# Performance work log

Hardware: AMD Instinct MI355X
Metric: run time of the kernel (lower is better)

The kernel has to match this reference:

```python
import jax, jax.numpy as jnp
import numpy as np

# --- model hyperparameters (match init_kwargs) ---
N_NODES = 128
IN_F = 3
H = 32            # hidden_node_size = output_node_size
HE = 64           # hidden_edge_size
OE = 32           # output_edge_size
N_MPS = 4
N_NODE_LAYERS = 2
ALPHA = 0.1       # leaky relu slope
E_IN = 2 * H + 2  # input_edge_size with intensity=True
BN_EPS = 1e-5


def _bn(x, gamma, beta):
    # BatchNorm1d in training mode: biased batch statistics over axis 0
    mu = jnp.mean(x, axis=0)
    var = jnp.var(x, axis=0)
    return gamma * (x - mu) * jax.lax.rsqrt(var + BN_EPS) + beta


def _lrelu(x):
    return jax.nn.leaky_relu(x, negative_slope=ALPHA)


def setup_inputs() -> dict:
    key = jax.random.key(0)
    ks = jax.random.split(key, 20)
    B = 64
    s = 0.05
    inp = {
        "x": jax.random.normal(ks[0], (B, N_NODES, IN_F), dtype=jnp.float32),
        # edge MLP (aggregate_hidden, aggregate), stacked over mp steps
        "Wah": jax.random.normal(ks[1], (N_MPS, E_IN, HE), dtype=jnp.float32) * s,
        "bah": jax.random.normal(ks[2], (N_MPS, HE), dtype=jnp.float32) * s,
        "Wa": jax.random.normal(ks[3], (N_MPS, HE, OE), dtype=jnp.float32) * s,
        "ba": jax.random.normal(ks[4], (N_MPS, OE), dtype=jnp.float32) * s,
        # edge batchnorm affine params
        "g_eh": jnp.ones((N_MPS, HE), dtype=jnp.float32),
        "b_eh": jnp.zeros((N_MPS, HE), dtype=jnp.float32),
        "g_e": jnp.ones((N_MPS, OE), dtype=jnp.float32),
        "b_e": jnp.zeros((N_MPS, OE), dtype=jnp.float32),
        # node update MLP: first layer (OE+H -> H), then (L-1) layers (H -> H)
        "Wn0": jax.random.normal(ks[5], (N_MPS, OE + H, H), dtype=jnp.float32) * s,
        "bn0": jax.random.normal(ks[6], (N_MPS, H), dtype=jnp.float32) * s,
        "Wn": jax.random.normal(ks[7], (N_MPS, N_NODE_LAYERS - 1, H, H), dtype=jnp.float32) * s,
        "bnn": jax.random.normal(ks[8], (N_MPS, N_NODE_LAYERS - 1, H), dtype=jnp.float32) * s,
        # node batchnorm affine params (one per node hidden layer)
        "g_n": jnp.ones((N_MPS, N_NODE_LAYERS, H), dtype=jnp.float32),
        "b_n": jnp.zeros((N_MPS, N_NODE_LAYERS, H), dtype=jnp.float32),
        # final update linear
        "Wu": jax.random.normal(ks[9], (N_MPS, H, H), dtype=jnp.float32) * s,
        "bu": jax.random.normal(ks[10], (N_MPS, H), dtype=jnp.float32) * s,
    }
    return inp


def reference(x, Wah, bah, Wa, ba, g_eh, b_eh, g_e, b_e, Wn0, bn0, Wn, bnn, g_n, b_n, Wu, bu):
    B, N, Fi = x.shape
    # pad input node features to hidden_node_size
    x = jnp.pad(x, ((0, 0), (0, 0), (0, H - Fi)))  # [B, N, H]
    for i in range(N_MPS):
        # dense all-pairs edge features: row (a,b) = [x_a, x_b, dist_ab, int_ab]
        x1 = jnp.broadcast_to(x[:, :, None, :], (B, N, N, H))  # sender varies on axis 1
        x2 = jnp.broadcast_to(x[:, None, :, :], (B, N, N, H))  # receiver varies on axis 2
        diff = x2[..., :-1] - x1[..., :-1] + 1e-12             # [B,N,N,H-1]
        dists = jnp.sqrt(jnp.sum(diff * diff, axis=-1, keepdims=True))
        int_diffs = 1.0 - (x2[..., -1:] - x1[..., -1:])
        A = jnp.concatenate([x1, x2, dists, int_diffs], axis=-1)
        A = A.reshape(B * N * N, E_IN)
        # edge MLP with batchnorm (training-mode stats); dropout p=0 (identity)
        A = _bn(_lrelu(A @ Wah[i] + bah[i]), g_eh[i], b_eh[i])
        A = _bn(_lrelu(A @ Wa[i] + ba[i]), g_e[i], b_e[i])
        # sum-aggregate over neighbors (axis 2)
        agg = jnp.sum(A.reshape(B, N, N, OE), axis=2)          # [B, N, OE]
        h = jnp.concatenate([agg, x], axis=-1).reshape(B * N, OE + H)
        # node update MLP
        h = _bn(_lrelu(h @ Wn0[i] + bn0[i]), g_n[i, 0], b_n[i, 0])
        for j in range(1, N_NODE_LAYERS):
            h = _bn(_lrelu(h @ Wn[i, j - 1] + bnn[i, j - 1]), g_n[i, j], b_n[i, j])
        x = jnp.tanh(h @ Wu[i] + bu[i]).reshape(B, N, H)
    return x
```

## Files before the change

kernel.cpp:

```cpp
#include <hip/hip_runtime.h>
#include <hip/hip_bf16.h>


#define ALPHA 0.1f
#define BN_EPS 1e-5f
#define LRELU(v) ((v) > 0.f ? (v) : ALPHA * (v))

typedef __attribute__((ext_vector_type(8))) short short8v;
typedef __attribute__((ext_vector_type(4))) float f32x4;

union U8 { short8v v; unsigned int u[4]; };

__device__ __forceinline__ unsigned short bf16rne(float f) {
    unsigned int u = __float_as_uint(f);
    unsigned int r = u + 0x7fffu + ((u >> 16) & 1u);
    return (unsigned short)(r >> 16);
}
__device__ __forceinline__ float bf16tof(unsigned short h) {
    return __uint_as_float(((unsigned int)h) << 16);
}
__device__ __forceinline__ void cvt8(const float* y, unsigned int* hu, unsigned int* lu) {
#pragma unroll
    for (int p = 0; p < 4; ++p) {
        unsigned int hpair;
        asm("v_cvt_pk_bf16_f32 %0, %1, %2" : "=v"(hpair) : "v"(y[2*p]), "v"(y[2*p+1]));
        const float h0 = __uint_as_float(hpair << 16);
        const float h1 = __uint_as_float(hpair & 0xffff0000u);
        unsigned int lpair;
        const float r0 = y[2*p] - h0;
        const float r1 = y[2*p+1] - h1;
        asm("v_cvt_pk_bf16_f32 %0, %1, %2" : "=v"(lpair) : "v"(r0), "v"(r1));
        hu[p] = hpair;
        lu[p] = lpair;
    }
}

__global__ __launch_bounds__(128) void k_pad_prep(const float* __restrict__ x,
                                                  const float* __restrict__ W1,
                                                  const float* __restrict__ b1,
                                                  float* __restrict__ xc,
                                                  float* __restrict__ P1,
                                                  float* __restrict__ P2,
                                                  float2* __restrict__ nbuf) {
    __shared__ float w1s[384];
    __shared__ float b1s[64];
    const int tid = threadIdx.x;
    for (int u = tid; u < 384; u += 128) {
        const int r = u >> 6, c = u & 63;
        const int srow = (r < 3) ? r : (32 + r - 3);
        w1s[u] = W1[srow * 64 + c];
    }
    if (tid < 64) b1s[tid] = b1[tid];
    const int row = blockIdx.x * 128 + tid;
    const float x0 = x[row * 3 + 0], x1 = x[row * 3 + 1], x2 = x[row * 3 + 2];
    __syncthreads();
    float4* xp = (float4*)(xc + row * 32);
    xp[0] = make_float4(x0, x1, x2, 0.f);
    const float4 z4 = make_float4(0.f, 0.f, 0.f, 0.f);
#pragma unroll
    for (int u = 1; u < 8; ++u) xp[u] = z4;
    nbuf[row] = make_float2(x0 * x0 + x1 * x1 + x2 * x2, 0.f);
    float* p1p = P1 + row * 64;
    float* p2p = P2 + row * 64;
#pragma unroll
    for (int c = 0; c < 64; ++c) {
        p1p[c] = b1s[c] + x0 * w1s[c] + x1 * w1s[64 + c] + x2 * w1s[128 + c];
        p2p[c] = x0 * w1s[192 + c] + x1 * w1s[256 + c] + x2 * w1s[320 + c];
    }
}

__global__ __launch_bounds__(256) void k_edge1(const float* __restrict__ xc,
                                               const float2* __restrict__ nbuf,
                                               const float* __restrict__ P1,
                                               const float* __restrict__ P2,
                                               const float* __restrict__ W1,
                                               float* __restrict__ stA) {
    __shared__ float xs[128 * 33];
    __shared__ float ddot[1024];
    __shared__ float2 nls[128];
    __shared__ float p1s[512];
    __shared__ float red[256];
    const int tid = threadIdx.x;
    const int b = blockIdx.x >> 4;
    const int ibase = (blockIdx.x & 15) * 8;
    const float* xg = xc + b * 4096;
    for (int u = tid; u < 4096; u += 256) xs[(u >> 5) * 33 + (u & 31)] = xg[u];
    if (tid < 128) nls[tid] = nbuf[b * 128 + tid];
    for (int u = tid; u < 512; u += 256)
        p1s[u] = P1[(b * 128 + ibase + (u >> 6)) * 64 + (u & 63)];
    __syncthreads();
    {
        const int il = tid >> 5, jb = tid & 31;
        const float* xi = &xs[(ibase + il) * 33];
        float xi_r[31];
#pragma unroll
        for (int k = 0; k < 31; ++k) xi_r[k] = xi[k];
        for (int q = 0; q < 4; ++q) {
            const int j = jb + 32 * q;
            const float* xj = &xs[j * 33];
            float d = 0.f;
#pragma unroll
            for (int k = 0; k < 31; ++k) d = fmaf(xi_r[k], xj[k], d);
            ddot[il * 128 + j] = d;
        }
    }
    __syncthreads();
    const int w = tid >> 6, l = tid & 63;
    const int tq = tid & 127;
    const int ch = (tid >> 7) * 32;
    const float2 nj = nls[tq];
    float4 p2v[8], wav[8], wbv[8];
    {
        const float* p2r = P2 + (b * 128 + tq) * 64 + ch;
        const float* war = W1 + 64 * 64 + ch;
        const float* wbr = W1 + 65 * 64 + ch;
#pragma unroll
        for (int u = 0; u < 8; ++u) {
            p2v[u] = *(const float4*)(p2r + u * 4);
            wav[u] = *(const float4*)(war + u * 4);
            wbv[u] = *(const float4*)(wbr + u * 4);
        }
    }
    float sum[32], sq[32];
#pragma unroll
    for (int k = 0; k < 32; ++k) { sum[k] = 0.f; sq[k] = 0.f; }
#pragma unroll 1
    for (int c = 0; c < 8; ++c) {
        const float2 ni = nls[ibase + c];
        const float dot = ddot[c * 128 + tq];
        const float dist = sqrtf(fmaxf(ni.x + nj.x - 2.f * dot, 0.f));
        const float itf = 1.f - (nj.y - ni.y);
        const float* p1r = &p1s[c * 64 + ch];
#pragma unroll
        for (int u = 0; u < 8; ++u) {
            const float4 p1v = *(const float4*)(p1r + u * 4);
            const float4 p2q = p2v[u];
            const float4 wa = wav[u];
            const float4 wb = wbv[u];
            float y0 = fmaf(itf, wb.x, fmaf(dist, wa.x, p1v.x + p2q.x));
            float y1 = fmaf(itf, wb.y, fmaf(dist, wa.y, p1v.y + p2q.y));
            float y2 = fmaf(itf, wb.z, fmaf(dist, wa.z, p1v.z + p2q.z));
            float y3 = fmaf(itf, wb.w, fmaf(dist, wa.w, p1v.w + p2q.w));
            y0 = LRELU(y0); y1 = LRELU(y1); y2 = LRELU(y2); y3 = LRELU(y3);
            sum[4*u+0] += y0; sq[4*u+0] += y0 * y0;
            sum[4*u+1] += y1; sq[4*u+1] += y1 * y1;
            sum[4*u+2] += y2; sq[4*u+2] += y2 * y2;
            sum[4*u+3] += y3; sq[4*u+3] += y3 * y3;
        }
    }
    {
        const int b5 = (l >> 5) & 1;
#pragma unroll
        for (int i = 0; i < 32; ++i) {
            const float keep = b5 ? sq[i] : sum[i];
            const float send = b5 ? sum[i] : sq[i];
            sum[i] = keep + __shfl_xor(send, 32, 64);
        }
        const int b4 = (l >> 4) & 1;
#pragma unroll
        for (int i = 0; i < 16; ++i) {
            const float keep = b4 ? sum[i + 16] : sum[i];
            const float send = b4 ? sum[i] : sum[i + 16];
            sum[i] = keep + __shfl_xor(send, 16, 64);
        }
        const int b3 = (l >> 3) & 1;
#pragma unroll
        for (int i = 0; i < 8; ++i) {
            const float keep = b3 ? sum[i + 8] : sum[i];
            const float send = b3 ? sum[i] : sum[i + 8];
            sum[i] = keep + __shfl_xor(send, 8, 64);
        }
        const int b2 = (l >> 2) & 1;
#pragma unroll
        for (int i = 0; i < 4; ++i) {
            const float keep = b2 ? sum[i + 4] : sum[i];
            const float send = b2 ? sum[i] : sum[i + 4];
            sum[i] = keep + __shfl_xor(send, 4, 64);
        }
        const int b1 = (l >> 1) & 1;
#pragma unroll
        for (int i = 0; i < 2; ++i) {
            const float keep = b1 ? sum[i + 2] : sum[i];
            const float send = b1 ? sum[i] : sum[i + 2];
            sum[i] = keep + __shfl_xor(send, 2, 64);
        }
        const int b0 = l & 1;
        {
            const float keep = b0 ? sum[1] : sum[0];
            const float send = b0 ? sum[0] : sum[1];
            sum[0] = keep + __shfl_xor(send, 1, 64);
        }
    }
    red[w * 64 + l] = sum[0];
    __syncthreads();
    if (tid < 128) {
        const int half = tid >> 6;
        const int l2 = tid & 63;
        const float val = red[half * 128 + l2] + red[half * 128 + 64 + l2];
        const int col = half * 32 + (l2 & 31);
        const int idx = (l2 < 32) ? col : (64 + col);
        atomicAdd(stA + idx, val);
    }
}

__global__ __launch_bounds__(256) void k_edge2(const float* __restrict__ xc,
                                               const float2* __restrict__ nbuf,
                                               const float* __restrict__ P1,
                                               const float* __restrict__ P2,
                                               const float* __restrict__ W1,
                                               const float* __restrict__ W2,
                                               const float* __restrict__ b2g,
                                               const float* __restrict__ g1,
                                               const float* __restrict__ bt1,
                                               const float* __restrict__ stA,
                                               float* __restrict__ stB,
                                               float* __restrict__ aggp) {
    __shared__ __align__(16) char smem_u[16896];
    __shared__ float ddot[1024];
    __shared__ float2 nls[128];
    __shared__ unsigned short wfbs[4096];
    __shared__ float s1s[64], t1s[64];
    __shared__ float p1s[512];
    __shared__ float part[256];
    __shared__ float b2ps[32];
    __shared__ float aggl[256];
    __shared__ float sqil[256];
    float* xs = (float*)smem_u;
    float* cbAll = (float*)smem_u;
    const int tid = threadIdx.x;
    const int b = blockIdx.x >> 4;
    const int ibase = (blockIdx.x & 15) * 8;
    const float* xg = xc + b * 4096;
    for (int u = tid; u < 4096; u += 256) xs[(u >> 5) * 33 + (u & 31)] = xg[u];
    if (tid < 128) nls[tid] = nbuf[b * 128 + tid];
    for (int u = tid; u < 512; u += 256)
        p1s[u] = P1[(b * 128 + ibase + (u >> 6)) * 64 + (u & 63)];
    if (tid < 64) {
        const float ic = 1.f / 1048576.f;
        const float mu = stA[tid] * ic;
        const float var = stA[64 + tid] * ic - mu * mu;
        const float sv = g1[tid] * rsqrtf(var + BN_EPS);
        s1s[tid] = sv;
        t1s[tid] = bt1[tid] - mu * sv;
    }
    __syncthreads();
    {
        const int il = tid >> 5, jb = tid & 31;
        const float* xi = &xs[(ibase + il) * 33];
        float xi_r[31];
#pragma unroll
        for (int k = 0; k < 31; ++k) xi_r[k] = xi[k];
        for (int q = 0; q < 4; ++q) {
            const int j = jb + 32 * q;
            const float* xj = &xs[j * 33];
            float d = 0.f;
#pragma unroll
            for (int k = 0; k < 31; ++k) d = fmaf(xi_r[k], xj[k], d);
            ddot[il * 128 + j] = d;
        }
    }
    {
        const int ks2n = tid >> 6, L = tid & 63;
        const int ks = ks2n >> 1, n = ks2n & 1;
#pragma unroll
        for (int e = 0; e < 8; ++e) {
            const int k = (L >> 4) * 8 + e + 32 * ks;
            const int col = n * 16 + (L & 15);
            const float wv = W2[k * 32 + col] * s1s[k];
            const unsigned short hi = bf16rne(wv);
            const unsigned short lo = bf16rne(wv - bf16tof(hi));
            wfbs[(ks2n * 64 + L) * 8 + e] = hi;
            wfbs[2048 + (ks2n * 64 + L) * 8 + e] = lo;
        }
    }
    {
        const int colp = tid & 31, kg2 = tid >> 5;
        float p = 0.f;
#pragma unroll
        for (int e = 0; e < 8; ++e) {
            const int k = kg2 * 8 + e;
            p = fmaf(t1s[k], W2[k * 32 + colp], p);
        }
        part[kg2 * 32 + colp] = p;
    }
    __syncthreads();
    if (tid < 32) {
        float acc = b2g[tid];
#pragma unroll
        for (int g = 0; g < 8; ++g) acc += part[g * 32 + tid];
        b2ps[tid] = acc;
    }
    const int w = tid >> 6, l = tid & 63;
    short8v bfh[2][2], bfl[2][2];
#pragma unroll
    for (int ks = 0; ks < 2; ++ks)
#pragma unroll
        for (int n = 0; n < 2; ++n) {
            bfh[ks][n] = *(const short8v*)(wfbs + ((ks * 2 + n) * 64 + l) * 8);
            bfl[ks][n] = *(const short8v*)(wfbs + 2048 + ((ks * 2 + n) * 64 + l) * 8);
        }
    __syncthreads();
    const float b2p0 = b2ps[l & 15];
    const float b2p1 = b2ps[16 + (l & 15)];
    const int kb = (l >> 4) * 8;
    const int lb4 = (l >> 4) & 1;
    const int lb5 = (l >> 5) & 1;
    const float* wab = W1 + 64 * 64;
    const float* wbb = W1 + 65 * 64;
    const float4 waA0 = *(const float4*)(wab + kb);
    const float4 waA1 = *(const float4*)(wab + kb + 4);
    const float4 waB0 = *(const float4*)(wab + 32 + kb);
    const float4 waB1 = *(const float4*)(wab + 32 + kb + 4);
    const float4 wbA0 = *(const float4*)(wbb + kb);
    const float4 wbA1 = *(const float4*)(wbb + kb + 4);
    const float4 wbB0 = *(const float4*)(wbb + 32 + kb);
    const float4 wbB1 = *(const float4*)(wbb + 32 + kb + 4);
    const int jrow0 = (w * 2 + 0) * 16 + (l & 15);
    const int jrow1 = (w * 2 + 1) * 16 + (l & 15);
    const float2 nj0 = nls[jrow0];
    const float2 nj1 = nls[jrow1];
    float4 p2r0v[4], p2r1v[4];
    {
        const float* p2b0 = P2 + (b * 128 + jrow0) * 64;
        const float* p2b1 = P2 + (b * 128 + jrow1) * 64;
        p2r0v[0] = *(const float4*)(p2b0 + kb);
        p2r0v[1] = *(const float4*)(p2b0 + kb + 4);
        p2r0v[2] = *(const float4*)(p2b0 + 32 + kb);
        p2r0v[3] = *(const float4*)(p2b0 + 32 + kb + 4);
        p2r1v[0] = *(const float4*)(p2b1 + kb);
        p2r1v[1] = *(const float4*)(p2b1 + kb + 4);
        p2r1v[2] = *(const float4*)(p2b1 + 32 + kb);
        p2r1v[3] = *(const float4*)(p2b1 + 32 + kb + 4);
    }

#pragma unroll 1
    for (int c = 0; c < 8; ++c) {
        const float2 ni = nls[ibase + c];
        const float* p1b = &p1s[c * 64];
        const float4 p1A0 = *(const float4*)(p1b + kb);
        const float4 p1A1 = *(const float4*)(p1b + kb + 4);
        const float4 p1B0 = *(const float4*)(p1b + 32 + kb);
        const float4 p1B1 = *(const float4*)(p1b + 32 + kb + 4);
        float accg = 0.f;
        {
            const float dot = ddot[c * 128 + jrow0];
            const float dist = sqrtf(fmaxf(ni.x + nj0.x - 2.f * dot, 0.f));
            const float itf = 1.f - (nj0.y - ni.y);
            const float4 p20 = p2r0v[0];
            const float4 p21 = p2r0v[1];
            const float4 p22 = p2r0v[2];
            const float4 p23 = p2r0v[3];
            float ya[8], yb[8];
            ya[0] = LRELU(fmaf(itf, wbA0.x, fmaf(dist, waA0.x, p1A0.x + p20.x)));
            ya[1] = LRELU(fmaf(itf, wbA0.y, fmaf(dist, waA0.y, p1A0.y + p20.y)));
            ya[2] = LRELU(fmaf(itf, wbA0.z, fmaf(dist, waA0.z, p1A0.z + p20.z)));
            ya[3] = LRELU(fmaf(itf, wbA0.w, fmaf(dist, waA0.w, p1A0.w + p20.w)));
            ya[4] = LRELU(fmaf(itf, wbA1.x, fmaf(dist, waA1.x, p1A1.x + p21.x)));
            ya[5] = LRELU(fmaf(itf, wbA1.y, fmaf(dist, waA1.y, p1A1.y + p21.y)));
            ya[6] = LRELU(fmaf(itf, wbA1.z, fmaf(dist, waA1.z, p1A1.z + p21.z)));
            ya[7] = LRELU(fmaf(itf, wbA1.w, fmaf(dist, waA1.w, p1A1.w + p21.w)));
            yb[0] = LRELU(fmaf(itf, wbB0.x, fmaf(dist, waB0.x, p1B0.x + p22.x)));
            yb[1] = LRELU(fmaf(itf, wbB0.y, fmaf(dist, waB0.y, p1B0.y + p22.y)));
            yb[2] = LRELU(fmaf(itf, wbB0.z, fmaf(dist, waB0.z, p1B0.z + p22.z)));
            yb[3] = LRELU(fmaf(itf, wbB0.w, fmaf(dist, waB0.w, p1B0.w + p22.w)));
            yb[4] = LRELU(fmaf(itf, wbB1.x, fmaf(dist, waB1.x, p1B1.x + p23.x)));
            yb[5] = LRELU(fmaf(itf, wbB1.y, fmaf(dist, waB1.y, p1B1.y + p23.y)));
            yb[6] = LRELU(fmaf(itf, wbB1.z, fmaf(dist, waB1.z, p1B1.z + p23.z)));
            yb[7] = LRELU(fmaf(itf, wbB1.w, fmaf(dist, waB1.w, p1B1.w + p23.w)));
            U8 a0h, a0l, a1h, a1l;
            cvt8(ya, a0h.u, a0l.u);
            cvt8(yb, a1h.u, a1l.u);
            f32x4 acc0 = {0.f, 0.f, 0.f, 0.f};
            f32x4 acc1 = {0.f, 0.f, 0.f, 0.f};
            acc0 = __builtin_amdgcn_mfma_f32_16x16x32_bf16(a0h.v, bfh[0][0], acc0, 0, 0, 0);
            acc0 = __builtin_amdgcn_mfma_f32_16x16x32_bf16(a0h.v, bfl[0][0], acc0, 0, 0, 0);
            acc0 = __builtin_amdgcn_mfma_f32_16x16x32_bf16(a0l.v, bfh[0][0], acc0, 0, 0, 0);
            acc0 = __builtin_amdgcn_mfma_f32_16x16x32_bf16(a1h.v, bfh[1][0], acc0, 0, 0, 0);
            acc0 = __builtin_amdgcn_mfma_f32_16x16x32_bf16(a1h.v, bfl[1][0], acc0, 0, 0, 0);
            acc0 = __builtin_amdgcn_mfma_f32_16x16x32_bf16(a1l.v, bfh[1][0], acc0, 0, 0, 0);
            acc1 = __builtin_amdgcn_mfma_f32_16x16x32_bf16(a0h.v, bfh[0][1], acc1, 0, 0, 0);
            acc1 = __builtin_amdgcn_mfma_f32_16x16x32_bf16(a0h.v, bfl[0][1], acc1, 0, 0, 0);
            acc1 = __builtin_amdgcn_mfma_f32_16x16x32_bf16(a0l.v, bfh[0][1], acc1, 0, 0, 0);
            acc1 = __builtin_amdgcn_mfma_f32_16x16x32_bf16(a1h.v, bfh[1][1], acc1, 0, 0, 0);
            acc1 = __builtin_amdgcn_mfma_f32_16x16x32_bf16(a1h.v, bfl[1][1], acc1, 0, 0, 0);
            acc1 = __builtin_amdgcn_mfma_f32_16x16x32_bf16(a1l.v, bfh[1][1], acc1, 0, 0, 0);
            float s0 = 0.f, q0 = 0.f, s1 = 0.f, q1 = 0.f;
#pragma unroll
            for (int r4 = 0; r4 < 4; ++r4) {
                const float z0 = LRELU(acc0[r4] + b2p0);
                const float z1 = LRELU(acc1[r4] + b2p1);
                s0 += z0; q0 += z0 * z0;
                s1 += z1; q1 += z1 * z1;
            }
            float sA = lb4 ? s1 : s0;
            float sB = lb4 ? s0 : s1;
            float qA = lb4 ? q1 : q0;
            float qB = lb4 ? q0 : q1;
            sA += __shfl_xor(sB, 16, 64);
            qA += __shfl_xor(qB, 16, 64);
            float vA = lb5 ? qA : sA;
            float vB = lb5 ? sA : qA;
            vA += __shfl_xor(vB, 32, 64);
            accg = vA;
        }
        {
            const float dot = ddot[c * 128 + jrow1];
            const float dist = sqrtf(fmaxf(ni.x + nj1.x - 2.f * dot, 0.f));
            const float itf = 1.f - (nj1.y - ni.y);
            const float4 p20 = p2r1v[0];
            const float4 p21 = p2r1v[1];
            const float4 p22 = p2r1v[2];
            const float4 p23 = p2r1v[3];
            float ya[8], yb[8];
            ya[0] = LRELU(fmaf(itf, wbA0.x, fmaf(dist, waA0.x, p1A0.x + p20.x)));
            ya[1] = LRELU(fmaf(itf, wbA0.y, fmaf(dist, waA0.y, p1A0.y + p20.y)));
            ya[2] = LRELU(fmaf(itf, wbA0.z, fmaf(dist, waA0.z, p1A0.z + p20.z)));
            ya[3] = LRELU(fmaf(itf, wbA0.w, fmaf(dist, waA0.w, p1A0.w + p20.w)));
            ya[4] = LRELU(fmaf(itf, wbA1.x, fmaf(dist, waA1.x, p1A1.x + p21.x)));
            ya[5] = LRELU(fmaf(itf, wbA1.y, fmaf(dist, waA1.y, p1A1.y + p21.y)));
            ya[6] = LRELU(fmaf(itf, wbA1.z, fmaf(dist, waA1.z, p1A1.z + p21.z)));
            ya[7] = LRELU(fmaf(itf, wbA1.w, fmaf(dist, waA1.w, p1A1.w + p21.w)));
            yb[0] = LRELU(fmaf(itf, wbB0.x, fmaf(dist, waB0.x, p1B0.x + p22.x)));
            yb[1] = LRELU(fmaf(itf, wbB0.y, fmaf(dist, waB0.y, p1B0.y + p22.y)));
            yb[2] = LRELU(fmaf(itf, wbB0.z, fmaf(dist, waB0.z, p1B0.z + p22.z)));
            yb[3] = LRELU(fmaf(itf, wbB0.w, fmaf(dist, waB0.w, p1B0.w + p22.w)));
            yb[4] = LRELU(fmaf(itf, wbB1.x, fmaf(dist, waB1.x, p1B1.x + p23.x)));
            yb[5] = LRELU(fmaf(itf, wbB1.y, fmaf(dist, waB1.y, p1B1.y + p23.y)));
            yb[6] = LRELU(fmaf(itf, wbB1.z, fmaf(dist, waB1.z, p1B1.z + p23.z)));
            yb[7] = LRELU(fmaf(itf, wbB1.w, fmaf(dist, waB1.w, p1B1.w + p23.w)));
            U8 a0h, a0l, a1h, a1l;
            cvt8(ya, a0h.u, a0l.u);
            cvt8(yb, a1h.u, a1l.u);
            f32x4 acc0 = {0.f, 0.f, 0.f, 0.f};
            f32x4 acc1 = {0.f, 0.f, 0.f, 0.f};
            acc0 = __builtin_amdgcn_mfma_f32_16x16x32_bf16(a0h.v, bfh[0][0], acc0, 0, 0, 0);
            acc0 = __builtin_amdgcn_mfma_f32_16x16x32_bf16(a0h.v, bfl[0][0], acc0, 0, 0, 0);
            acc0 = __builtin_amdgcn_mfma_f32_16x16x32_bf16(a0l.v, bfh[0][0], acc0, 0, 0, 0);
            acc0 = __builtin_amdgcn_mfma_f32_16x16x32_bf16(a1h.v, bfh[1][0], acc0, 0, 0, 0);
            acc0 = __builtin_amdgcn_mfma_f32_16x16x32_bf16(a1h.v, bfl[1][0], acc0, 0, 0, 0);
            acc0 = __builtin_amdgcn_mfma_f32_16x16x32_bf16(a1l.v, bfh[1][0], acc0, 0, 0, 0);
            acc1 = __builtin_amdgcn_mfma_f32_16x16x32_bf16(a0h.v, bfh[0][1], acc1, 0, 0, 0);
            acc1 = __builtin_amdgcn_mfma_f32_16x16x32_bf16(a0h.v, bfl[0][1], acc1, 0, 0, 0);
            acc1 = __builtin_amdgcn_mfma_f32_16x16x32_bf16(a0l.v, bfh[0][1], acc1, 0, 0, 0);
            acc1 = __builtin_amdgcn_mfma_f32_16x16x32_bf16(a1h.v, bfh[1][1], acc1, 0, 0, 0);
            acc1 = __builtin_amdgcn_mfma_f32_16x16x32_bf16(a1h.v, bfl[1][1], acc1, 0, 0, 0);
            acc1 = __builtin_amdgcn_mfma_f32_16x16x32_bf16(a1l.v, bfh[1][1], acc1, 0, 0, 0);
            float s0 = 0.f, q0 = 0.f, s1 = 0.f, q1 = 0.f;
#pragma unroll
            for (int r4 = 0; r4 < 4; ++r4) {
                const float z0 = LRELU(acc0[r4] + b2p0);
                const float z1 = LRELU(acc1[r4] + b2p1);
                s0 += z0; q0 += z0 * z0;
                s1 += z1; q1 += z1 * z1;
            }
            float sA = lb4 ? s1 : s0;
            float sB = lb4 ? s0 : s1;
            float qA = lb4 ? q1 : q0;
            float qB = lb4 ? q0 : q1;
            sA += __shfl_xor(sB, 16, 64);
            qA += __shfl_xor(qB, 16, 64);
            float vA = lb5 ? qA : sA;
            float vB = lb5 ? sA : qA;
            vA += __shfl_xor(vB, 32, 64);
            accg += vA;
        }
        cbAll[c * 256 + w * 64 + lb5 * 32 + lb4 * 16 + (l & 15)] = accg;
    }
    __syncthreads();
    {
        const int c2 = tid >> 5, col = tid & 31;
        const float* base = cbAll + c2 * 256;
        const float s = base[col] + base[64 + col] + base[128 + col] + base[192 + col];
        const float qq = base[32 + col] + base[96 + col] + base[160 + col] + base[224 + col];
        aggp[(b * 128 + ibase + c2) * 32 + col] = s;
        aggl[c2 * 32 + col] = s;
        sqil[c2 * 32 + col] = qq;
    }
    __syncthreads();
    if (tid < 32) {
        float s = 0.f, qq = 0.f;
#pragma unroll
        for (int il3 = 0; il3 < 8; ++il3) { s += aggl[il3 * 32 + tid]; qq += sqil[il3 * 32 + tid]; }
        atomicAdd(stB + tid, s);
        atomicAdd(stB + 32 + tid, qq);
    }
}

__device__ __forceinline__ void gbar(unsigned int* ctr, unsigned int target) {
    __syncthreads();
    if (threadIdx.x == 0) {
        __hip_atomic_fetch_add(ctr, 1u, __ATOMIC_ACQ_REL, __HIP_MEMORY_SCOPE_AGENT);
        while (__hip_atomic_load(ctr, __ATOMIC_ACQUIRE, __HIP_MEMORY_SCOPE_AGENT) < target) {
            __builtin_amdgcn_s_sleep(2);
        }
    }
    __syncthreads();
}

__global__ __launch_bounds__(256) void k_nodeF(
    const float* __restrict__ aggp, const float* __restrict__ xc,
    const float* __restrict__ W0, const float* __restrict__ b0,
    const float* __restrict__ stB, const float* __restrict__ g2, const float* __restrict__ bt2,
    const float* __restrict__ W1m, const float* __restrict__ b1m,
    float* __restrict__ stC, const float* __restrict__ gC, const float* __restrict__ btC,
    const float* __restrict__ W2m, const float* __restrict__ b2m,
    float* __restrict__ stD, const float* __restrict__ gD, const float* __restrict__ btD,
    float* __restrict__ xout,
    const float* __restrict__ W1n, const float* __restrict__ b1n,
    float* __restrict__ P1, float* __restrict__ P2, float2* __restrict__ nbuf,
    unsigned int* __restrict__ bar, int doPrep)
{
    __shared__ float w0s[2048];
    __shared__ float wms[1024];
    __shared__ float wus[1024];
    __shared__ float w1s[4096];
    __shared__ float b0s[32], s2s[32], t2s[32];
    __shared__ float bms[32], sCs[32], tCs[32];
    __shared__ float bus[32], sDs[32], tDs[32];
    __shared__ float b1s[64];
    __shared__ float red[256];
    const int tid = threadIdx.x;
    const int row = blockIdx.x * 256 + tid;
    for (int k = tid; k < 2048; k += 256) w0s[k] = W0[k];
    for (int k = tid; k < 1024; k += 256) { wms[k] = W1m[k]; wus[k] = W2m[k]; }
    if (doPrep) {
        for (int k = tid; k < 4096; k += 256) w1s[k] = W1n[k];
        if (tid < 64) b1s[tid] = b1n[tid];
    }
    if (tid < 32) {
        b0s[tid] = b0[tid]; bms[tid] = b1m[tid]; bus[tid] = b2m[tid];
        const float ic = 1.f / 1048576.f;
        const float mu = stB[tid] * ic;
        const float var = stB[32 + tid] * ic - mu * mu;
        const float sv = g2[tid] * rsqrtf(var + BN_EPS);
        s2s[tid] = sv; t2s[tid] = bt2[tid] - mu * sv;
    }
    __syncthreads();
    float h[64];
    {
        const float4* ap = (const float4*)(aggp + row * 32);
        const float4* xp = (const float4*)(xc + row * 32);
#pragma unroll
        for (int u = 0; u < 8; ++u) {
            const float4 a = ap[u];
            h[4*u+0] = fmaf(s2s[4*u+0], a.x, 128.f * t2s[4*u+0]);
            h[4*u+1] = fmaf(s2s[4*u+1], a.y, 128.f * t2s[4*u+1]);
            h[4*u+2] = fmaf(s2s[4*u+2], a.z, 128.f * t2s[4*u+2]);
            h[4*u+3] = fmaf(s2s[4*u+3], a.w, 128.f * t2s[4*u+3]);
            const float4 xv = xp[u];
            h[32+4*u+0] = xv.x; h[32+4*u+1] = xv.y; h[32+4*u+2] = xv.z; h[32+4*u+3] = xv.w;
        }
    }
    float v[32];
#pragma unroll
    for (int o0 = 0; o0 < 32; o0 += 4) {
        float z0 = b0s[o0], z1 = b0s[o0+1], z2 = b0s[o0+2], z3 = b0s[o0+3];
#pragma unroll
        for (int k = 0; k < 64; ++k) {
            const float4 wv = *(const float4*)&w0s[k * 32 + o0];
            const float hv = h[k];
            z0 = fmaf(hv, wv.x, z0); z1 = fmaf(hv, wv.y, z1);
            z2 = fmaf(hv, wv.z, z2); z3 = fmaf(hv, wv.w, z3);
        }
        v[o0] = LRELU(z0); v[o0+1] = LRELU(z1); v[o0+2] = LRELU(z2); v[o0+3] = LRELU(z3);
    }
    {
        float sarr[32], qarr[32];
#pragma unroll
        for (int o = 0; o < 32; ++o) {
            float s = v[o], q = v[o] * v[o];
#pragma unroll
            for (int m = 1; m < 64; m <<= 1) { s += __shfl_xor(s, m, 64); q += __shfl_xor(q, m, 64); }
            sarr[o] = s; qarr[o] = q;
        }
        const int lane = tid & 63, wid = tid >> 6;
        if (lane == 0) {
#pragma unroll
            for (int o = 0; o < 32; ++o) { red[wid * 64 + o] = sarr[o]; red[wid * 64 + 32 + o] = qarr[o]; }
        }
        __syncthreads();
        if (tid < 64) {
            const float t = red[tid] + red[64 + tid] + red[128 + tid] + red[192 + tid];
            atomicAdd(stC + tid, t);
        }
    }
    gbar(bar + 0, 32);
    if (tid < 32) {
        const float ic = 1.f / 8192.f;
        const float mu = __hip_atomic_load(stC + tid, __ATOMIC_RELAXED, __HIP_MEMORY_SCOPE_AGENT) * ic;
        const float sq = __hip_atomic_load(stC + 32 + tid, __ATOMIC_RELAXED, __HIP_MEMORY_SCOPE_AGENT) * ic;
        const float var = sq - mu * mu;
        const float sv = gC[tid] * rsqrtf(var + BN_EPS);
        sCs[tid] = sv; tCs[tid] = btC[tid] - mu * sv;
    }
    __syncthreads();
    float hh[32];
#pragma unroll
    for (int c = 0; c < 32; ++c) hh[c] = fmaf(sCs[c], v[c], tCs[c]);
    float v2[32];
#pragma unroll
    for (int o0 = 0; o0 < 32; o0 += 4) {
        float z0 = bms[o0], z1 = bms[o0+1], z2 = bms[o0+2], z3 = bms[o0+3];
#pragma unroll
        for (int k = 0; k < 32; ++k) {
            const float4 wv = *(const float4*)&wms[k * 32 + o0];
            const float hv = hh[k];
            z0 = fmaf(hv, wv.x, z0); z1 = fmaf(hv, wv.y, z1);
            z2 = fmaf(hv, wv.z, z2); z3 = fmaf(hv, wv.w, z3);
        }
        v2[o0] = LRELU(z0); v2[o0+1] = LRELU(z1); v2[o0+2] = LRELU(z2); v2[o0+3] = LRELU(z3);
    }
    {
        float sarr[32], qarr[32];
#pragma unroll
        for (int o = 0; o < 32; ++o) {
            float s = v2[o], q = v2[o] * v2[o];
#pragma unroll
            for (int m = 1; m < 64; m <<= 1) { s += __shfl_xor(s, m, 64); q += __shfl_xor(q, m, 64); }
            sarr[o] = s; qarr[o] = q;
        }
        const int lane = tid & 63, wid = tid >> 6;
        __syncthreads();
        if (lane == 0) {
#pragma unroll
            for (int o = 0; o < 32; ++o) { red[wid * 64 + o] = sarr[o]; red[wid * 64 + 32 + o] = qarr[o]; }
        }
        __syncthreads();
        if (tid < 64) {
            const float t = red[tid] + red[64 + tid] + red[128 + tid] + red[192 + tid];
            atomicAdd(stD + tid, t);
        }
    }
    gbar(bar + 1, 32);
    if (tid < 32) {
        const float ic = 1.f / 8192.f;
        const float mu = __hip_atomic_load(stD + tid, __ATOMIC_RELAXED, __HIP_MEMORY_SCOPE_AGENT) * ic;
        const float sq = __hip_atomic_load(stD + 32 + tid, __ATOMIC_RELAXED, __HIP_MEMORY_SCOPE_AGENT) * ic;
        const float var = sq - mu * mu;
        const float sv = gD[tid] * rsqrtf(var + BN_EPS);
        sDs[tid] = sv; tDs[tid] = btD[tid] - mu * sv;
    }
    __syncthreads();
    float h3[32];
#pragma unroll
    for (int c = 0; c < 32; ++c) h3[c] = fmaf(sDs[c], v2[c], tDs[c]);
    float xn[32];
    float* xp = xout + row * 32;
#pragma unroll
    for (int o0 = 0; o0 < 32; o0 += 4) {
        float z0 = bus[o0], z1 = bus[o0+1], z2 = bus[o0+2], z3 = bus[o0+3];
#pragma unroll
        for (int k = 0; k < 32; ++k) {
            const float4 wv = *(const float4*)&wus[k * 32 + o0];
            const float hv = h3[k];
            z0 = fmaf(hv, wv.x, z0); z1 = fmaf(hv, wv.y, z1);
            z2 = fmaf(hv, wv.z, z2); z3 = fmaf(hv, wv.w, z3);
        }
        xn[o0]   = tanhf(z0);
        xn[o0+1] = tanhf(z1);
        xn[o0+2] = tanhf(z2);
        xn[o0+3] = tanhf(z3);
        xp[o0] = xn[o0]; xp[o0+1] = xn[o0+1]; xp[o0+2] = xn[o0+2]; xp[o0+3] = xn[o0+3];
    }
    if (!doPrep) return;
    float n = 0.f;
#pragma unroll
    for (int k = 0; k < 31; ++k) n = fmaf(xn[k], xn[k], n);
    nbuf[row] = make_float2(n, xn[31]);
    float* p1p = P1 + row * 64;
    float* p2p = P2 + row * 64;
#pragma unroll
    for (int c0 = 0; c0 < 64; c0 += 4) {
        float a0 = b1s[c0], a1 = b1s[c0+1], a2 = b1s[c0+2], a3 = b1s[c0+3];
        float q0 = 0.f, q1 = 0.f, q2 = 0.f, q3 = 0.f;
#pragma unroll
        for (int k = 0; k < 32; ++k) {
            const float xv = xn[k];
            const float4 wa = *(const float4*)&w1s[k * 64 + c0];
            const float4 wb = *(const float4*)&w1s[(32 + k) * 64 + c0];
            a0 = fmaf(xv, wa.x, a0); a1 = fmaf(xv, wa.y, a1);
            a2 = fmaf(xv, wa.z, a2); a3 = fmaf(xv, wa.w, a3);
            q0 = fmaf(xv, wb.x, q0); q1 = fmaf(xv, wb.y, q1);
            q2 = fmaf(xv, wb.z, q2); q3 = fmaf(xv, wb.w, q3);
        }
        p1p[c0] = a0; p1p[c0+1] = a1; p1p[c0+2] = a2; p1p[c0+3] = a3;
        p2p[c0] = q0; p2p[c0+1] = q1; p2p[c0+2] = q2; p2p[c0+3] = q3;
    }
}

extern "C" void kernel_launch(void* const* d_in, const int* in_sizes, int n_in,
                              void* d_out, int out_size, void* d_ws, size_t ws_size,
                              hipStream_t stream) {
    const float* x    = (const float*)d_in[0];
    const float* Wah  = (const float*)d_in[1];
    const float* bah  = (const float*)d_in[2];
    const float* Wa   = (const float*)d_in[3];
    const float* ba   = (const float*)d_in[4];
    const float* g_eh = (const float*)d_in[5];
    const float* b_eh = (const float*)d_in[6];
    const float* g_e  = (const float*)d_in[7];
    const float* b_e  = (const float*)d_in[8];
    const float* Wn0  = (const float*)d_in[9];
    const float* bn0  = (const float*)d_in[10];
    const float* Wn   = (const float*)d_in[11];
    const float* bnn  = (const float*)d_in[12];
    const float* g_n  = (const float*)d_in[13];
    const float* b_n  = (const float*)d_in[14];
    const float* Wu   = (const float*)d_in[15];
    const float* bu   = (const float*)d_in[16];

    float* ws    = (float*)d_ws;
    float* xc    = ws;
    float* aggp  = ws + 262144;
    float* P1    = ws + 786432;
    float* P2    = ws + 1310720;
    float2* nbuf = (float2*)(ws + 1835008);
    float* stats = ws + 1867776;
    unsigned int* bar = (unsigned int*)(ws + 1869056);
    float* out   = (float*)d_out;

    hipMemsetAsync(stats, 0, (1280 + 16) * sizeof(float), stream);
    k_pad_prep<<<64, 128, 0, stream>>>(x, Wah, bah, xc, P1, P2, nbuf);

    for (int s = 0; s < 4; ++s) {
        const float* W1 = Wah + s * 66 * 64;
        const float* W2 = Wa + s * 64 * 32;
        const float* b2 = ba + s * 32;
        float* stA = stats + s * 320;
        float* stB = stA + 128;
        float* stC = stA + 192;
        float* stD = stA + 256;

        k_edge1<<<1024, 256, 0, stream>>>(xc, nbuf, P1, P2, W1, stA);
        k_edge2<<<1024, 256, 0, stream>>>(xc, nbuf, P1, P2, W1, W2, b2,
                                          g_eh + s * 64, b_eh + s * 64, stA, stB, aggp);
        k_nodeF<<<32, 256, 0, stream>>>(aggp, xc, Wn0 + s * 2048, bn0 + s * 32,
                                        stB, g_e + s * 32, b_e + s * 32,
                                        Wn + s * 1024, bnn + s * 32,
                                        stC, g_n + s * 64, b_n + s * 64,
                                        Wu + s * 1024, bu + s * 32,
                                        stD, g_n + s * 64 + 32, b_n + s * 64 + 32,
                                        (s == 3) ? out : xc,
                                        (s < 3) ? (Wah + (s + 1) * 66 * 64) : Wah,
                                        (s < 3) ? (bah + (s + 1) * 64) : bah,
                                        P1, P2, nbuf, bar + s * 2, (s < 3) ? 1 : 0);
    }
}
```

Baseline: 536.8 us.

## Split node kernel into 128 single-wave blocks with transpose-style butterfly reduction

The node-update kernel now launches 128 blocks of 64 threads instead of 32 blocks of 256, spreading the 8192 rows across more CUs. The per-column sum and sum-of-squares reduction is replaced by a recursive-halving butterfly across the wave, so each lane ends holding one of the 64 statistics. This cuts shuffles from 64×6 to 63 per lane and removes the shared-memory stage. In exchange, the grid barrier must now wait for 128 blocks and there are 4× more global atomics per stat. Each block also reloads the full weight set into LDS.

```diff
diff --git a/kernel.cpp b/kernel.cpp
--- a/kernel.cpp
+++ b/kernel.cpp
@@ -497,7 +497,7 @@
     __syncthreads();
 }
 
-__global__ __launch_bounds__(256) void k_nodeF(
+__global__ __launch_bounds__(64) void k_nodeF(
     const float* __restrict__ aggp, const float* __restrict__ xc,
     const float* __restrict__ W0, const float* __restrict__ b0,
     const float* __restrict__ stB, const float* __restrict__ g2, const float* __restrict__ bt2,
@@ -518,14 +518,13 @@
     __shared__ float bms[32], sCs[32], tCs[32];
     __shared__ float bus[32], sDs[32], tDs[32];
     __shared__ float b1s[64];
-    __shared__ float red[256];
     const int tid = threadIdx.x;
-    const int row = blockIdx.x * 256 + tid;
-    for (int k = tid; k < 2048; k += 256) w0s[k] = W0[k];
-    for (int k = tid; k < 1024; k += 256) { wms[k] = W1m[k]; wus[k] = W2m[k]; }
+    const int row = blockIdx.x * 64 + tid;
+    for (int k = tid; k < 2048; k += 64) w0s[k] = W0[k];
+    for (int k = tid; k < 1024; k += 64) { wms[k] = W1m[k]; wus[k] = W2m[k]; }
     if (doPrep) {
-        for (int k = tid; k < 4096; k += 256) w1s[k] = W1n[k];
-        if (tid < 64) b1s[tid] = b1n[tid];
+        for (int k = tid; k < 4096; k += 64) w1s[k] = W1n[k];
+        b1s[tid] = b1n[tid];
     }
     if (tid < 32) {
         b0s[tid] = b0[tid]; bms[tid] = b1m[tid]; bus[tid] = b2m[tid];
@@ -565,26 +564,53 @@
         v[o0] = LRELU(z0); v[o0+1] = LRELU(z1); v[o0+2] = LRELU(z2); v[o0+3] = LRELU(z3);
     }
     {
-        float sarr[32], qarr[32];
-#pragma unroll
-        for (int o = 0; o < 32; ++o) {
-            float s = v[o], q = v[o] * v[o];
-#pragma unroll
-            for (int m = 1; m < 64; m <<= 1) { s += __shfl_xor(s, m, 64); q += __shfl_xor(q, m, 64); }
-            sarr[o] = s; qarr[o] = q;
-        }
-        const int lane = tid & 63, wid = tid >> 6;
-        if (lane == 0) {
-#pragma unroll
-            for (int o = 0; o < 32; ++o) { red[wid * 64 + o] = sarr[o]; red[wid * 64 + 32 + o] = qarr[o]; }
-        }
-        __syncthreads();
-        if (tid < 64) {
-            const float t = red[tid] + red[64 + tid] + red[128 + tid] + red[192 + tid];
-            atomicAdd(stC + tid, t);
-        }
-    }
-    gbar(bar + 0, 32);
+        float su[32], qu[32];
+#pragma unroll
+        for (int o = 0; o < 32; ++o) { su[o] = v[o]; qu[o] = v[o] * v[o]; }
+        const int b5 = (tid >> 5) & 1;
+#pragma unroll
+        for (int i = 0; i < 32; ++i) {
+            const float keep = b5 ? qu[i] : su[i];
+            const float send = b5 ? su[i] : qu[i];
+            su[i] = keep + __shfl_xor(send, 32, 64);
+        }
+        const int b4 = (tid >> 4) & 1;
+#pragma unroll
+        for (int i = 0; i < 16; ++i) {
+            const float keep = b4 ? su[i + 16] : su[i];
+            const float send = b4 ? su[i] : su[i + 16];
+            su[i] = keep + __shfl_xor(send, 16, 64);
+        }
+        const int b3 = (tid >> 3) & 1;
+#pragma unroll
+        for (int i = 0; i < 8; ++i) {
+            const float keep = b3 ? su[i + 8] : su[i];
+            const float send = b3 ? su[i] : su[i + 8];
+            su[i] = keep + __shfl_xor(send, 8, 64);
+        }
+        const int b2 = (tid >> 2) & 1;
+#pragma unroll
+        for (int i = 0; i < 4; ++i) {
+            const float keep = b2 ? su[i + 4] : su[i];
+            const float send = b2 ? su[i] : su[i + 4];
+            su[i] = keep + __shfl_xor(send, 4, 64);
+        }
+        const int b1 = (tid >> 1) & 1;
+#pragma unroll
+        for (int i = 0; i < 2; ++i) {
+            const float keep = b1 ? su[i + 2] : su[i];
+            const float send = b1 ? su[i] : su[i + 2];
+            su[i] = keep + __shfl_xor(send, 2, 64);
+        }
+        const int b0b = tid & 1;
+        {
+            const float keep = b0b ? su[1] : su[0];
+            const float send = b0b ? su[0] : su[1];
+            su[0] = keep + __shfl_xor(send, 1, 64);
+        }
+        atomicAdd(stC + tid, su[0]);
+    }
+    gbar(bar + 0, 128);
     if (tid < 32) {
         const float ic = 1.f / 8192.f;
         const float mu = __hip_atomic_load(stC + tid, __ATOMIC_RELAXED, __HIP_MEMORY_SCOPE_AGENT) * ic;
@@ -611,27 +637,53 @@
         v2[o0] = LRELU(z0); v2[o0+1] = LRELU(z1); v2[o0+2] = LRELU(z2); v2[o0+3] = LRELU(z3);
     }
     {
-        float sarr[32], qarr[32];
-#pragma unroll
-        for (int o = 0; o < 32; ++o) {
-            float s = v2[o], q = v2[o] * v2[o];
-#pragma unroll
-            for (int m = 1; m < 64; m <<= 1) { s += __shfl_xor(s, m, 64); q += __shfl_xor(q, m, 64); }
-            sarr[o] = s; qarr[o] = q;
-        }
-        const int lane = tid & 63, wid = tid >> 6;
-        __syncthreads();
-        if (lane == 0) {
-#pragma unroll
-            for (int o = 0; o < 32; ++o) { red[wid * 64 + o] = sarr[o]; red[wid * 64 + 32 + o] = qarr[o]; }
-        }
-        __syncthreads();
-        if (tid < 64) {
-            const float t = red[tid] + red[64 + tid] + red[128 + tid] + red[192 + tid];
-            atomicAdd(stD + tid, t);
-        }
-    }
-    gbar(bar + 1, 32);
+        float su[32], qu[32];
+#pragma unroll
+        for (int o = 0; o < 32; ++o) { su[o] = v2[o]; qu[o] = v2[o] * v2[o]; }
+        const int b5 = (tid >> 5) & 1;
+#pragma unroll
+        for (int i = 0; i < 32; ++i) {
+            const float keep = b5 ? qu[i] : su[i];
+            const float send = b5 ? su[i] : qu[i];
+            su[i] = keep + __shfl_xor(send, 32, 64);
+        }
+        const int b4 = (tid >> 4) & 1;
+#pragma unroll
+        for (int i = 0; i < 16; ++i) {
+            const float keep = b4 ? su[i + 16] : su[i];
+            const float send = b4 ? su[i] : su[i + 16];
+            su[i] = keep + __shfl_xor(send, 16, 64);
+        }
+        const int b3 = (tid >> 3) & 1;
+#pragma unroll
+        for (int i = 0; i < 8; ++i) {
+            const float keep = b3 ? su[i + 8] : su[i];
+            const float send = b3 ? su[i] : su[i + 8];
+            su[i] = keep + __shfl_xor(send, 8, 64);
+        }
+        const int b2 = (tid >> 2) & 1;
+#pragma unroll
+        for (int i = 0; i < 4; ++i) {
+            const float keep = b2 ? su[i + 4] : su[i];
+            const float send = b2 ? su[i] : su[i + 4];
+            su[i] = keep + __shfl_xor(send, 4, 64);
+        }
+        const int b1 = (tid >> 1) & 1;
+#pragma unroll
+        for (int i = 0; i < 2; ++i) {
+            const float keep = b1 ? su[i + 2] : su[i];
+            const float send = b1 ? su[i] : su[i + 2];
+            su[i] = keep + __shfl_xor(send, 2, 64);
+        }
+        const int b0b = tid & 1;
+        {
+            const float keep = b0b ? su[1] : su[0];
+            const float send = b0b ? su[0] : su[1];
+            su[0] = keep + __shfl_xor(send, 1, 64);
+        }
+        atomicAdd(stD + tid, su[0]);
+    }
+    gbar(bar + 1, 128);
     if (tid < 32) {
         const float ic = 1.f / 8192.f;
         const float mu = __hip_atomic_load(stD + tid, __ATOMIC_RELAXED, __HIP_MEMORY_SCOPE_AGENT) * ic;
@@ -734,7 +786,7 @@
         k_edge1<<<1024, 256, 0, stream>>>(xc, nbuf, P1, P2, W1, stA);
         k_edge2<<<1024, 256, 0, stream>>>(xc, nbuf, P1, P2, W1, W2, b2,
                                           g_eh + s * 64, b_eh + s * 64, stA, stB, aggp);
-        k_nodeF<<<32, 256, 0, stream>>>(aggp, xc, Wn0 + s * 2048, bn0 + s * 32,
+        k_nodeF<<<128, 64, 0, stream>>>(aggp, xc, Wn0 + s * 2048, bn0 + s * 32,
                                         stB, g_e + s * 32, b_e + s * 32,
                                         Wn + s * 1024, bnn + s * 32,
                                         stC, g_n + s * 64, b_n + s * 64,
```

Result: no change. 542.4 us (+1.0%).

## Split each node row across four threads and launch four times more node blocks

Applied to the files above, without the earlier changes.

The fused node-update kernel now assigns each row to a group of four threads, each computing 8 output columns, and launches 128 blocks instead of 32. Full hidden vectors are rebuilt with intra-wave shuffles between layers. Batch-norm statistics are reduced with shorter shuffle trees before the atomics, and stores become float4. The aim is more CUs and more latency hiding for this serial per-row MLP chain. The cost is extra shuffles, redundant input loads, and a grid barrier that now spans 128 co-resident blocks.

```diff
diff --git a/kernel.cpp b/kernel.cpp
--- a/kernel.cpp
+++ b/kernel.cpp
@@ -520,7 +520,11 @@
     __shared__ float b1s[64];
     __shared__ float red[256];
     const int tid = threadIdx.x;
-    const int row = blockIdx.x * 256 + tid;
+    const int l = tid & 63, w = tid >> 6;
+    const int part = tid & 3;
+    const int row = blockIdx.x * 64 + (tid >> 2);
+    const int ob = part * 8;
+    const int gbase = l & ~3;
     for (int k = tid; k < 2048; k += 256) w0s[k] = W0[k];
     for (int k = tid; k < 1024; k += 256) { wms[k] = W1m[k]; wus[k] = W2m[k]; }
     if (doPrep) {
@@ -551,9 +555,10 @@
             h[32+4*u+0] = xv.x; h[32+4*u+1] = xv.y; h[32+4*u+2] = xv.z; h[32+4*u+3] = xv.w;
         }
     }
-    float v[32];
-#pragma unroll
-    for (int o0 = 0; o0 < 32; o0 += 4) {
+    float v[8];
+#pragma unroll
+    for (int oo = 0; oo < 8; oo += 4) {
+        const int o0 = ob + oo;
         float z0 = b0s[o0], z1 = b0s[o0+1], z2 = b0s[o0+2], z3 = b0s[o0+3];
 #pragma unroll
         for (int k = 0; k < 64; ++k) {
@@ -562,29 +567,32 @@
             z0 = fmaf(hv, wv.x, z0); z1 = fmaf(hv, wv.y, z1);
             z2 = fmaf(hv, wv.z, z2); z3 = fmaf(hv, wv.w, z3);
         }
-        v[o0] = LRELU(z0); v[o0+1] = LRELU(z1); v[o0+2] = LRELU(z2); v[o0+3] = LRELU(z3);
-    }
-    {
-        float sarr[32], qarr[32];
-#pragma unroll
-        for (int o = 0; o < 32; ++o) {
-            float s = v[o], q = v[o] * v[o];
-#pragma unroll
-            for (int m = 1; m < 64; m <<= 1) { s += __shfl_xor(s, m, 64); q += __shfl_xor(q, m, 64); }
-            sarr[o] = s; qarr[o] = q;
-        }
-        const int lane = tid & 63, wid = tid >> 6;
-        if (lane == 0) {
-#pragma unroll
-            for (int o = 0; o < 32; ++o) { red[wid * 64 + o] = sarr[o]; red[wid * 64 + 32 + o] = qarr[o]; }
-        }
-        __syncthreads();
-        if (tid < 64) {
-            const float t = red[tid] + red[64 + tid] + red[128 + tid] + red[192 + tid];
-            atomicAdd(stC + tid, t);
-        }
-    }
-    gbar(bar + 0, 32);
+        v[oo] = LRELU(z0); v[oo+1] = LRELU(z1); v[oo+2] = LRELU(z2); v[oo+3] = LRELU(z3);
+    }
+    {
+        float st[16];
+#pragma unroll
+        for (int i = 0; i < 8; ++i) { st[i] = v[i]; st[8 + i] = v[i] * v[i]; }
+#pragma unroll
+        for (int m = 4; m <= 32; m <<= 1) {
+#pragma unroll
+            for (int i = 0; i < 16; ++i) st[i] += __shfl_xor(st[i], m, 64);
+        }
+        if (l < 4) {
+#pragma unroll
+            for (int i = 0; i < 16; ++i) red[w * 64 + (l & 3) * 16 + i] = st[i];
+        }
+    }
+    __syncthreads();
+    if (tid < 64) {
+        const float val = red[tid] + red[64 + tid] + red[128 + tid] + red[192 + tid];
+        const int p2i = tid >> 4;
+        const int ii = tid & 15;
+        const int col = p2i * 8 + (ii & 7);
+        const int isq = (ii >> 3) & 1;
+        atomicAdd(stC + isq * 32 + col, val);
+    }
+    gbar(bar + 0, 128);
     if (tid < 32) {
         const float ic = 1.f / 8192.f;
         const float mu = __hip_atomic_load(stC + tid, __ATOMIC_RELAXED, __HIP_MEMORY_SCOPE_AGENT) * ic;
@@ -595,11 +603,20 @@
     }
     __syncthreads();
     float hh[32];
-#pragma unroll
-    for (int c = 0; c < 32; ++c) hh[c] = fmaf(sCs[c], v[c], tCs[c]);
-    float v2[32];
-#pragma unroll
-    for (int o0 = 0; o0 < 32; o0 += 4) {
+    {
+#pragma unroll
+        for (int g = 0; g < 4; ++g) {
+#pragma unroll
+            for (int i = 0; i < 8; ++i) {
+                const float val = __shfl(v[i], gbase + g, 64);
+                hh[g * 8 + i] = fmaf(sCs[g * 8 + i], val, tCs[g * 8 + i]);
+            }
+        }
+    }
+    float v2[8];
+#pragma unroll
+    for (int oo = 0; oo < 8; oo += 4) {
+        const int o0 = ob + oo;
         float z0 = bms[o0], z1 = bms[o0+1], z2 = bms[o0+2], z3 = bms[o0+3];
 #pragma unroll
         for (int k = 0; k < 32; ++k) {
@@ -608,30 +625,33 @@
             z0 = fmaf(hv, wv.x, z0); z1 = fmaf(hv, wv.y, z1);
             z2 = fmaf(hv, wv.z, z2); z3 = fmaf(hv, wv.w, z3);
         }
-        v2[o0] = LRELU(z0); v2[o0+1] = LRELU(z1); v2[o0+2] = LRELU(z2); v2[o0+3] = LRELU(z3);
-    }
-    {
-        float sarr[32], qarr[32];
-#pragma unroll
-        for (int o = 0; o < 32; ++o) {
-            float s = v2[o], q = v2[o] * v2[o];
-#pragma unroll
-            for (int m = 1; m < 64; m <<= 1) { s += __shfl_xor(s, m, 64); q += __shfl_xor(q, m, 64); }
-            sarr[o] = s; qarr[o] = q;
-        }
-        const int lane = tid & 63, wid = tid >> 6;
+        v2[oo] = LRELU(z0); v2[oo+1] = LRELU(z1); v2[oo+2] = LRELU(z2); v2[oo+3] = LRELU(z3);
+    }
+    {
+        float st[16];
+#pragma unroll
+        for (int i = 0; i < 8; ++i) { st[i] = v2[i]; st[8 + i] = v2[i] * v2[i]; }
+#pragma unroll
+        for (int m = 4; m <= 32; m <<= 1) {
+#pragma unroll
+            for (int i = 0; i < 16; ++i) st[i] += __shfl_xor(st[i], m, 64);
+        }
         __syncthreads();
-        if (lane == 0) {
-#pragma unroll
-            for (int o = 0; o < 32; ++o) { red[wid * 64 + o] = sarr[o]; red[wid * 64 + 32 + o] = qarr[o]; }
-        }
-        __syncthreads();
-        if (tid < 64) {
-            const float t = red[tid] + red[64 + tid] + red[128 + tid] + red[192 + tid];
-            atomicAdd(stD + tid, t);
-        }
-    }
-    gbar(bar + 1, 32);
+        if (l < 4) {
+#pragma unroll
+            for (int i = 0; i < 16; ++i) red[w * 64 + (l & 3) * 16 + i] = st[i];
+        }
+    }
+    __syncthreads();
+    if (tid < 64) {
+        const float val = red[tid] + red[64 + tid] + red[128 + tid] + red[192 + tid];
+        const int p2i = tid >> 4;
+        const int ii = tid & 15;
+        const int col = p2i * 8 + (ii & 7);
+        const int isq = (ii >> 3) & 1;
+        atomicAdd(stD + isq * 32 + col, val);
+    }
+    gbar(bar + 1, 128);
     if (tid < 32) {
         const float ic = 1.f / 8192.f;
         const float mu = __hip_atomic_load(stD + tid, __ATOMIC_RELAXED, __HIP_MEMORY_SCOPE_AGENT) * ic;
@@ -642,12 +662,20 @@
     }
     __syncthreads();
     float h3[32];
-#pragma unroll
-    for (int c = 0; c < 32; ++c) h3[c] = fmaf(sDs[c], v2[c], tDs[c]);
-    float xn[32];
-    float* xp = xout + row * 32;
-#pragma unroll
-    for (int o0 = 0; o0 < 32; o0 += 4) {
+    {
+#pragma unroll
+        for (int g = 0; g < 4; ++g) {
+#pragma unroll
+            for (int i = 0; i < 8; ++i) {
+                const float val = __shfl(v2[i], gbase + g, 64);
+                h3[g * 8 + i] = fmaf(sDs[g * 8 + i], val, tDs[g * 8 + i]);
+            }
+        }
+    }
+    float xn[8];
+#pragma unroll
+    for (int oo = 0; oo < 8; oo += 4) {
+        const int o0 = ob + oo;
         float z0 = bus[o0], z1 = bus[o0+1], z2 = bus[o0+2], z3 = bus[o0+3];
 #pragma unroll
         for (int k = 0; k < 32; ++k) {
@@ -656,35 +684,53 @@
             z0 = fmaf(hv, wv.x, z0); z1 = fmaf(hv, wv.y, z1);
             z2 = fmaf(hv, wv.z, z2); z3 = fmaf(hv, wv.w, z3);
         }
-        xn[o0]   = tanhf(z0);
-        xn[o0+1] = tanhf(z1);
-        xn[o0+2] = tanhf(z2);
-        xn[o0+3] = tanhf(z3);
-        xp[o0] = xn[o0]; xp[o0+1] = xn[o0+1]; xp[o0+2] = xn[o0+2]; xp[o0+3] = xn[o0+3];
+        xn[oo]   = tanhf(z0);
+        xn[oo+1] = tanhf(z1);
+        xn[oo+2] = tanhf(z2);
+        xn[oo+3] = tanhf(z3);
+    }
+    {
+        float* xp = xout + row * 32 + ob;
+        *(float4*)(xp)     = make_float4(xn[0], xn[1], xn[2], xn[3]);
+        *(float4*)(xp + 4) = make_float4(xn[4], xn[5], xn[6], xn[7]);
     }
     if (!doPrep) return;
-    float n = 0.f;
-#pragma unroll
-    for (int k = 0; k < 31; ++k) n = fmaf(xn[k], xn[k], n);
-    nbuf[row] = make_float2(n, xn[31]);
-    float* p1p = P1 + row * 64;
-    float* p2p = P2 + row * 64;
-#pragma unroll
-    for (int c0 = 0; c0 < 64; c0 += 4) {
-        float a0 = b1s[c0], a1 = b1s[c0+1], a2 = b1s[c0+2], a3 = b1s[c0+3];
+    float xnf[32];
+    {
+#pragma unroll
+        for (int g = 0; g < 4; ++g) {
+#pragma unroll
+            for (int i = 0; i < 8; ++i) {
+                xnf[g * 8 + i] = __shfl(xn[i], gbase + g, 64);
+            }
+        }
+    }
+    if (part == 0) {
+        float n = 0.f;
+#pragma unroll
+        for (int k = 0; k < 31; ++k) n = fmaf(xnf[k], xnf[k], n);
+        nbuf[row] = make_float2(n, xnf[31]);
+    }
+    const int cb = part * 16;
+    float* p1p = P1 + row * 64 + cb;
+    float* p2p = P2 + row * 64 + cb;
+#pragma unroll
+    for (int c0 = 0; c0 < 16; c0 += 4) {
+        const int col = cb + c0;
+        float a0 = b1s[col], a1 = b1s[col+1], a2 = b1s[col+2], a3 = b1s[col+3];
         float q0 = 0.f, q1 = 0.f, q2 = 0.f, q3 = 0.f;
 #pragma unroll
         for (int k = 0; k < 32; ++k) {
-            const float xv = xn[k];
-            const float4 wa = *(const float4*)&w1s[k * 64 + c0];
-            const float4 wb = *(const float4*)&w1s[(32 + k) * 64 + c0];
+            const float xv = xnf[k];
+            const float4 wa = *(const float4*)&w1s[k * 64 + col];
+            const float4 wb = *(const float4*)&w1s[(32 + k) * 64 + col];
             a0 = fmaf(xv, wa.x, a0); a1 = fmaf(xv, wa.y, a1);
             a2 = fmaf(xv, wa.z, a2); a3 = fmaf(xv, wa.w, a3);
             q0 = fmaf(xv, wb.x, q0); q1 = fmaf(xv, wb.y, q1);
             q2 = fmaf(xv, wb.z, q2); q3 = fmaf(xv, wb.w, q3);
         }
-        p1p[c0] = a0; p1p[c0+1] = a1; p1p[c0+2] = a2; p1p[c0+3] = a3;
-        p2p[c0] = q0; p2p[c0+1] = q1; p2p[c0+2] = q2; p2p[c0+3] = q3;
+        *(float4*)(p1p + c0) = make_float4(a0, a1, a2, a3);
+        *(float4*)(p2p + c0) = make_float4(q0, q1, q2, q3);
     }
 }
 
@@ -734,7 +780,7 @@
         k_edge1<<<1024, 256, 0, stream>>>(xc, nbuf, P1, P2, W1, stA);
         k_edge2<<<1024, 256, 0, stream>>>(xc, nbuf, P1, P2, W1, W2, b2,
                                           g_eh + s * 64, b_eh + s * 64, stA, stB, aggp);
-        k_nodeF<<<32, 256, 0, stream>>>(aggp, xc, Wn0 + s * 2048, bn0 + s * 32,
+        k_nodeF<<<128, 256, 0, stream>>>(aggp, xc, Wn0 + s * 2048, bn0 + s * 32,
                                         stB, g_e + s * 32, b_e + s * 32,
                                         Wn + s * 1024, bnn + s * 32,
                                         stC, g_n + s * 64, b_n + s * 64,
```

Measured after the change: 471.0 us. -12.3%, faster.
